# Optimization experiments

Measured on AMD Instinct MI355X. Metric: run time of the kernel, lower is better.

## Reference

```python
import jax, jax.numpy as jnp
import numpy as np

FEAT = 128 * 4 * 4   # 2048, from input_size=(64,128,4,4)
NCLS = 20            # hard-coded n_classes
S = 0.31             # threshold margin from forward()


def setup_inputs() -> dict:
    key = jax.random.key(0)
    kx, ke, kc, kf = jax.random.split(key, 4)
    x = jax.random.normal(kx, (16384, 128, 4, 4), dtype=jnp.float32)
    # encoder stub: linear 2048 -> 2048
    W_enc = jax.random.normal(ke, (FEAT, FEAT), dtype=jnp.float32) * 0.02
    b_enc = jnp.zeros((FEAT,), dtype=jnp.float32)
    # classifier: linear 2048 -> 20
    W_cls = jax.random.normal(kc, (FEAT, NCLS), dtype=jnp.float32) * 0.02
    b_cls = jnp.zeros((NCLS,), dtype=jnp.float32)
    # flow classification head: linear 2048 -> 20 (produces flow_logits)
    W_fl = jax.random.normal(kf, (FEAT, NCLS), dtype=jnp.float32) * 0.02
    b_fl = jnp.zeros((NCLS,), dtype=jnp.float32)
    return {"x": x, "W_enc": W_enc, "b_enc": b_enc,
            "W_cls": W_cls, "b_cls": b_cls, "W_fl": W_fl, "b_fl": b_fl}


def reference(x, W_enc, b_enc, W_cls, b_cls, W_fl, b_fl):
    B = x.shape[0]
    h = x.reshape(B, -1) @ W_enc + b_enc                    # encoder -> [B, 2048]
    cls_preds = jax.nn.softmax(h @ W_cls + b_cls, axis=1)   # [B, 20]
    flow_logits = h @ W_fl + b_fl                           # flow classify head, [B, 20]
    # taus = softmax(flow_logits).min(1); per-row confidence threshold
    tau = jnp.min(jax.nn.softmax(flow_logits, axis=1), axis=1)  # [B]
    predicted = jnp.max(cls_preds, axis=1)                      # [B]
    # original loop: if predicted < tau + s -> zero the row (vectorized here)
    keep = predicted >= tau + S
    return jnp.where(keep[:, None], cls_preds, jnp.zeros((), cls_preds.dtype))
```

## Files before the change

### kernel.cpp

```cpp
#include <hip/hip_runtime.h>
#include <math.h>


#define KD    2048
#define NROWS 16384
#define NCLS  20
#define NC2   40
#define SMARG 0.31f

#define WCAT_OFF 0
#define WEFF_OFF 81920
#define BIAS_OFF 163840

#define XS_STR  65
#define XS_BUF  (64 * XS_STR)
#define HACC_STR 41
#define HACC_WS  (64 * HACC_STR)
#define SMEM_FLOATS (8 * HACC_WS)

__global__ __launch_bounds__(256)
void k0_prep(const float* __restrict__ Wc, const float* __restrict__ bc,
             const float* __restrict__ Wf, const float* __restrict__ bf,
             const float* __restrict__ be, float* __restrict__ ws)
{
    const int b = blockIdx.x;
    const int t = threadIdx.x;
    if (b < 320) {
        const int idx = b * 256 + t;
        const int n = idx / NC2, c = idx % NC2;
        ws[WCAT_OFF + idx] = (c < NCLS) ? Wc[n * NCLS + c] : Wf[n * NCLS + (c - NCLS)];
        ws[WEFF_OFF + idx] = 0.f;
    } else {
        const int col = b - 320;
        const float* Wp = (col < NCLS) ? Wc : Wf;
        const int cc = (col < NCLS) ? col : col - NCLS;
        float p = 0.f;
        for (int n = t; n < KD; n += 256)
            p = fmaf(be[n], Wp[n * NCLS + cc], p);
        __shared__ float red[256];
        red[t] = p;
        __syncthreads();
        for (int s = 128; s > 0; s >>= 1) {
            if (t < s) red[t] += red[t + s];
            __syncthreads();
        }
        if (t == 0)
            ws[BIAS_OFF + col] = red[0] + ((col < NCLS) ? bc[cc] : bf[cc]);
    }
}

template<int NCHUNKS, bool FUSED>
__global__ __launch_bounds__(1024)
void skinny_gemm(const float* __restrict__ A,
                 const float* __restrict__ Bw,
                 float* __restrict__ Cacc,
                 const float* __restrict__ bias2,
                 float* __restrict__ outp)
{
    __shared__ float smem[SMEM_FLOATS];
    const int tid  = threadIdx.x;
    const int lane = tid & 63;
    const int wu   = __builtin_amdgcn_readfirstlane(tid >> 6);
    const int cgu  = wu & 1;
    const int ksu  = wu >> 1;
    const int ksub = ksu * 8;

    int m0, kbase;
    if (FUSED) { m0 = blockIdx.x * 64;        kbase = 0; }
    else       { m0 = (blockIdx.x >> 2) * 64; kbase = (blockIdx.x & 3) * (NCHUNKS * 64); }

    const int lrow = tid >> 4;
    const int lkq  = tid & 15;
    const float* aptr = A + (size_t)(m0 + lrow) * KD + kbase + 4 * lkq;

    float acc[20];
    #pragma unroll
    for (int j = 0; j < 20; ++j) acc[j] = 0.f;

    float4 v = *(const float4*)(aptr);
    {
        float* xb = smem;
        xb[(4 * lkq + 0) * XS_STR + lrow] = v.x;
        xb[(4 * lkq + 1) * XS_STR + lrow] = v.y;
        xb[(4 * lkq + 2) * XS_STR + lrow] = v.z;
        xb[(4 * lkq + 3) * XS_STR + lrow] = v.w;
    }
    __syncthreads();

    for (int c = 0; c < NCHUNKS; ++c) {
        const int buf = c & 1;
        if (c + 1 < NCHUNKS)
            v = *(const float4*)(aptr + (c + 1) * 64);

        const float* xs   = smem + buf * XS_BUF;
        const float* brow = Bw + (size_t)(kbase + c * 64 + ksub) * NC2 + 20 * cgu;
        #pragma unroll 4
        for (int kk = 0; kk < 8; ++kk) {
            float x = xs[(ksub + kk) * XS_STR + lane];
            #pragma unroll
            for (int j = 0; j < 20; ++j)
                acc[j] = fmaf(x, brow[kk * NC2 + j], acc[j]);
        }

        if (c + 1 < NCHUNKS) {
            float* xb = smem + (buf ^ 1) * XS_BUF;
            xb[(4 * lkq + 0) * XS_STR + lrow] = v.x;
            xb[(4 * lkq + 1) * XS_STR + lrow] = v.y;
            xb[(4 * lkq + 2) * XS_STR + lrow] = v.z;
            xb[(4 * lkq + 3) * XS_STR + lrow] = v.w;
        }
        __syncthreads();
    }

    float* H = smem;
    #pragma unroll
    for (int j = 0; j < 20; ++j)
        H[ksu * HACC_WS + lane * HACC_STR + 20 * cgu + j] = acc[j];
    __syncthreads();

    if (FUSED) {
        if (tid < 64) {
            float l[NC2];
            #pragma unroll
            for (int cc = 0; cc < NC2; ++cc) {
                float s = 0.f;
                #pragma unroll
                for (int ks = 0; ks < 8; ++ks)
                    s += H[ks * HACC_WS + tid * HACC_STR + cc];
                l[cc] = s + bias2[cc];
            }
            float mC = l[0];
            #pragma unroll
            for (int cc = 1; cc < NCLS; ++cc) mC = fmaxf(mC, l[cc]);
            float sC = 0.f;
            #pragma unroll
            for (int cc = 0; cc < NCLS; ++cc) sC += expf(l[cc] - mC);
            float mF = l[NCLS], mnF = l[NCLS];
            #pragma unroll
            for (int cc = NCLS + 1; cc < NC2; ++cc) {
                float vv = l[cc];
                mF = fmaxf(mF, vv);
                mnF = fminf(mnF, vv);
            }
            float sF = 0.f;
            #pragma unroll
            for (int cc = NCLS; cc < NC2; ++cc) sF += expf(l[cc] - mF);
            float pred  = 1.f / sC;
            float tau   = expf(mnF - mF) / sF;
            float scale = (pred >= tau + SMARG) ? pred : 0.f;
            float* op = outp + (size_t)(m0 + tid) * NCLS;
            #pragma unroll
            for (int cc = 0; cc < NCLS; ++cc)
                op[cc] = expf(l[cc] - mC) * scale;
        }
    } else {
        for (int idx = tid; idx < 64 * NC2; idx += 1024) {
            int row = idx / NC2, cc = idx % NC2;
            float s = 0.f;
            #pragma unroll
            for (int ks = 0; ks < 8; ++ks)
                s += H[ks * HACC_WS + row * HACC_STR + cc];
            atomicAdd(Cacc + (size_t)(m0 + row) * NC2 + cc, s);
        }
    }
}

extern "C" void kernel_launch(void* const* d_in, const int* in_sizes, int n_in,
                              void* d_out, int out_size, void* d_ws, size_t ws_size,
                              hipStream_t stream) {
    const float* X  = (const float*)d_in[0];
    const float* We = (const float*)d_in[1];
    const float* be = (const float*)d_in[2];
    const float* Wc = (const float*)d_in[3];
    const float* bc = (const float*)d_in[4];
    const float* Wf = (const float*)d_in[5];
    const float* bf = (const float*)d_in[6];
    float* out = (float*)d_out;
    float* ws  = (float*)d_ws;
    (void)in_sizes; (void)n_in; (void)out_size; (void)ws_size;

    k0_prep<<<dim3(360), dim3(256), 0, stream>>>(Wc, bc, Wf, bf, be, ws);
    skinny_gemm<8, false><<<dim3(128), dim3(1024), 0, stream>>>(
        We, ws + WCAT_OFF, ws + WEFF_OFF, nullptr, nullptr);
    skinny_gemm<32, true><<<dim3(256), dim3(1024), 0, stream>>>(
        X, ws + WEFF_OFF, nullptr, ws + BIAS_OFF, out);
}
```

Baseline: 239.6 us.

## Widen skinny GEMM chunks, use packed FMA and row-major LDS tiles

The skinny GEMM now processes 128-wide K chunks with a row-major X tile in LDS, read back as float4 vectors. Accumulation uses packed two-wide FMA on 2-float vectors. The prep kernel no longer builds a concatenated Wc/Wf copy: the first GEMM reads Wc and Wf directly through two base pointers, and the weight-fold GEMM is split 8-way over K across 256 blocks. The softmax epilogue and the output stores are vectorised. The aim is fewer LDS instructions, fewer global loads per FMA and higher FMA throughput, at the cost of more registers and a larger LDS footprint.

```diff
diff --git a/kernel.cpp b/kernel.cpp
--- a/kernel.cpp
+++ b/kernel.cpp
@@ -2,21 +2,31 @@
 #include <math.h>
 
 
+typedef float v2f __attribute__((ext_vector_type(2)));
+typedef float v4f __attribute__((ext_vector_type(4)));
+
 #define KD    2048
-#define NROWS 16384
 #define NCLS  20
 #define NC2   40
 #define SMARG 0.31f
 
-#define WCAT_OFF 0
-#define WEFF_OFF 81920
-#define BIAS_OFF 163840
-
-#define XS_STR  65
+#define WEFF_OFF 0
+#define BIAS_OFF 81920
+
+#define CHUNK   128
+#define XS_STR  132
 #define XS_BUF  (64 * XS_STR)
-#define HACC_STR 41
+#define HACC_STR 44
 #define HACC_WS  (64 * HACC_STR)
-#define SMEM_FLOATS (8 * HACC_WS)
+#define SMEM_FLOATS 22528
+
+static __device__ __forceinline__ v2f fma2(v2f a, v2f b, v2f c) {
+#if __has_builtin(__builtin_elementwise_fma)
+    return __builtin_elementwise_fma(a, b, c);
+#else
+    v2f r; r[0] = fmaf(a[0], b[0], c[0]); r[1] = fmaf(a[1], b[1], c[1]); return r;
+#endif
+}
 
 __global__ __launch_bounds__(256)
 void k0_prep(const float* __restrict__ Wc, const float* __restrict__ bc,
@@ -25,13 +35,11 @@
 {
     const int b = blockIdx.x;
     const int t = threadIdx.x;
-    if (b < 320) {
-        const int idx = b * 256 + t;
-        const int n = idx / NC2, c = idx % NC2;
-        ws[WCAT_OFF + idx] = (c < NCLS) ? Wc[n * NCLS + c] : Wf[n * NCLS + (c - NCLS)];
-        ws[WEFF_OFF + idx] = 0.f;
+    if (b < 80) {
+        v4f z = {0.f, 0.f, 0.f, 0.f};
+        *(v4f*)&ws[WEFF_OFF + 4 * (b * 256 + t)] = z;
     } else {
-        const int col = b - 320;
+        const int col = b - 80;
         const float* Wp = (col < NCLS) ? Wc : Wf;
         const int cc = (col < NCLS) ? col : col - NCLS;
         float p = 0.f;
@@ -49,109 +57,139 @@
     }
 }
 
-template<int NCHUNKS, bool FUSED>
+template<int NCHUNKS, int BSTR, bool FUSED>
 __global__ __launch_bounds__(1024)
 void skinny_gemm(const float* __restrict__ A,
-                 const float* __restrict__ Bw,
+                 const float* __restrict__ B0,
+                 const float* __restrict__ B1,
                  float* __restrict__ Cacc,
                  const float* __restrict__ bias2,
                  float* __restrict__ outp)
 {
-    __shared__ float smem[SMEM_FLOATS];
+    __shared__ __align__(16) float smem[SMEM_FLOATS];
     const int tid  = threadIdx.x;
     const int lane = tid & 63;
     const int wu   = __builtin_amdgcn_readfirstlane(tid >> 6);
     const int cgu  = wu & 1;
     const int ksu  = wu >> 1;
-    const int ksub = ksu * 8;
 
     int m0, kbase;
     if (FUSED) { m0 = blockIdx.x * 64;        kbase = 0; }
-    else       { m0 = (blockIdx.x >> 2) * 64; kbase = (blockIdx.x & 3) * (NCHUNKS * 64); }
+    else       { m0 = (blockIdx.x >> 3) * 64; kbase = (blockIdx.x & 7) * (NCHUNKS * CHUNK); }
 
     const int lrow = tid >> 4;
     const int lkq  = tid & 15;
-    const float* aptr = A + (size_t)(m0 + lrow) * KD + kbase + 4 * lkq;
-
-    float acc[20];
+    const float* aptr  = A + (size_t)(m0 + lrow) * KD + kbase + 4 * lkq;
+    const float* bbase = (cgu ? B1 : B0) + (size_t)(kbase + ksu * (CHUNK / 8)) * BSTR;
+
+    v2f acc[10];
     #pragma unroll
-    for (int j = 0; j < 20; ++j) acc[j] = 0.f;
-
-    float4 v = *(const float4*)(aptr);
+    for (int j = 0; j < 10; ++j) acc[j] = (v2f){0.f, 0.f};
+
     {
-        float* xb = smem;
-        xb[(4 * lkq + 0) * XS_STR + lrow] = v.x;
-        xb[(4 * lkq + 1) * XS_STR + lrow] = v.y;
-        xb[(4 * lkq + 2) * XS_STR + lrow] = v.z;
-        xb[(4 * lkq + 3) * XS_STR + lrow] = v.w;
+        v4f v0 = *(const v4f*)(aptr);
+        v4f v1 = *(const v4f*)(aptr + 64);
+        float* xb = smem + lrow * XS_STR;
+        *(v4f*)(xb + 4 * lkq)      = v0;
+        *(v4f*)(xb + 64 + 4 * lkq) = v1;
     }
     __syncthreads();
 
     for (int c = 0; c < NCHUNKS; ++c) {
         const int buf = c & 1;
-        if (c + 1 < NCHUNKS)
-            v = *(const float4*)(aptr + (c + 1) * 64);
-
-        const float* xs   = smem + buf * XS_BUF;
-        const float* brow = Bw + (size_t)(kbase + c * 64 + ksub) * NC2 + 20 * cgu;
-        #pragma unroll 4
-        for (int kk = 0; kk < 8; ++kk) {
-            float x = xs[(ksub + kk) * XS_STR + lane];
-            #pragma unroll
-            for (int j = 0; j < 20; ++j)
-                acc[j] = fmaf(x, brow[kk * NC2 + j], acc[j]);
-        }
-
+        v4f p0, p1;
         if (c + 1 < NCHUNKS) {
-            float* xb = smem + (buf ^ 1) * XS_BUF;
-            xb[(4 * lkq + 0) * XS_STR + lrow] = v.x;
-            xb[(4 * lkq + 1) * XS_STR + lrow] = v.y;
-            xb[(4 * lkq + 2) * XS_STR + lrow] = v.z;
-            xb[(4 * lkq + 3) * XS_STR + lrow] = v.w;
+            p0 = *(const v4f*)(aptr + (c + 1) * CHUNK);
+            p1 = *(const v4f*)(aptr + (c + 1) * CHUNK + 64);
+        }
+
+        const float* xs   = smem + buf * XS_BUF + lane * XS_STR + ksu * (CHUNK / 8);
+        const float* brow = bbase + (size_t)c * (CHUNK * BSTR);
+        #pragma unroll 2
+        for (int q = 0; q < 4; ++q) {
+            v4f xv = *(const v4f*)(xs + 4 * q);
+            #pragma unroll
+            for (int i = 0; i < 4; ++i) {
+                v2f xx = { xv[i], xv[i] };
+                const float* br = brow + (4 * q + i) * BSTR;
+                #pragma unroll
+                for (int j = 0; j < 10; ++j)
+                    acc[j] = fma2(xx, *(const v2f*)(br + 2 * j), acc[j]);
+            }
+        }
+
+        if (c + 1 < NCHUNKS) {
+            float* xb = smem + (buf ^ 1) * XS_BUF + lrow * XS_STR;
+            *(v4f*)(xb + 4 * lkq)      = p0;
+            *(v4f*)(xb + 64 + 4 * lkq) = p1;
         }
         __syncthreads();
     }
 
     float* H = smem;
-    #pragma unroll
-    for (int j = 0; j < 20; ++j)
-        H[ksu * HACC_WS + lane * HACC_STR + 20 * cgu + j] = acc[j];
+    {
+        float* Hw = H + ksu * HACC_WS + lane * HACC_STR + 20 * cgu;
+        #pragma unroll
+        for (int j = 0; j < 10; ++j)
+            *(v2f*)(Hw + 2 * j) = acc[j];
+    }
     __syncthreads();
 
     if (FUSED) {
         if (tid < 64) {
-            float l[NC2];
-            #pragma unroll
-            for (int cc = 0; cc < NC2; ++cc) {
-                float s = 0.f;
-                #pragma unroll
-                for (int ks = 0; ks < 8; ++ks)
-                    s += H[ks * HACC_WS + tid * HACC_STR + cc];
-                l[cc] = s + bias2[cc];
-            }
-            float mC = l[0];
-            #pragma unroll
-            for (int cc = 1; cc < NCLS; ++cc) mC = fmaxf(mC, l[cc]);
+            v4f l4[10];
+            #pragma unroll
+            for (int j = 0; j < 10; ++j) {
+                v4f s = *(const v4f*)(H + tid * HACC_STR + 4 * j);
+                #pragma unroll
+                for (int ks = 1; ks < 8; ++ks)
+                    s += *(const v4f*)(H + ks * HACC_WS + tid * HACC_STR + 4 * j);
+                l4[j] = s + *(const v4f*)(bias2 + 4 * j);
+            }
+            float mC = l4[0][0];
+            #pragma unroll
+            for (int j = 0; j < 5; ++j) {
+                #pragma unroll
+                for (int i = 0; i < 4; ++i) mC = fmaxf(mC, l4[j][i]);
+            }
+            float e[20];
             float sC = 0.f;
             #pragma unroll
-            for (int cc = 0; cc < NCLS; ++cc) sC += expf(l[cc] - mC);
-            float mF = l[NCLS], mnF = l[NCLS];
-            #pragma unroll
-            for (int cc = NCLS + 1; cc < NC2; ++cc) {
-                float vv = l[cc];
-                mF = fmaxf(mF, vv);
-                mnF = fminf(mnF, vv);
+            for (int j = 0; j < 5; ++j) {
+                #pragma unroll
+                for (int i = 0; i < 4; ++i) {
+                    float ev = expf(l4[j][i] - mC);
+                    e[4 * j + i] = ev;
+                    sC += ev;
+                }
+            }
+            float mF = l4[5][0], mnF = l4[5][0];
+            #pragma unroll
+            for (int j = 5; j < 10; ++j) {
+                #pragma unroll
+                for (int i = 0; i < 4; ++i) {
+                    float vv = l4[j][i];
+                    mF = fmaxf(mF, vv);
+                    mnF = fminf(mnF, vv);
+                }
             }
             float sF = 0.f;
             #pragma unroll
-            for (int cc = NCLS; cc < NC2; ++cc) sF += expf(l[cc] - mF);
+            for (int j = 5; j < 10; ++j) {
+                #pragma unroll
+                for (int i = 0; i < 4; ++i) sF += expf(l4[j][i] - mF);
+            }
             float pred  = 1.f / sC;
             float tau   = expf(mnF - mF) / sF;
             float scale = (pred >= tau + SMARG) ? pred : 0.f;
             float* op = outp + (size_t)(m0 + tid) * NCLS;
             #pragma unroll
-            for (int cc = 0; cc < NCLS; ++cc)
-                op[cc] = expf(l[cc] - mC) * scale;
+            for (int j = 0; j < 5; ++j) {
+                v4f o;
+                #pragma unroll
+                for (int i = 0; i < 4; ++i) o[i] = e[4 * j + i] * scale;
+                *(v4f*)(op + 4 * j) = o;
+            }
         }
     } else {
         for (int idx = tid; idx < 64 * NC2; idx += 1024) {
@@ -179,9 +217,9 @@
     float* ws  = (float*)d_ws;
     (void)in_sizes; (void)n_in; (void)out_size; (void)ws_size;
 
-    k0_prep<<<dim3(360), dim3(256), 0, stream>>>(Wc, bc, Wf, bf, be, ws);
-    skinny_gemm<8, false><<<dim3(128), dim3(1024), 0, stream>>>(
-        We, ws + WCAT_OFF, ws + WEFF_OFF, nullptr, nullptr);
-    skinny_gemm<32, true><<<dim3(256), dim3(1024), 0, stream>>>(
-        X, ws + WEFF_OFF, nullptr, ws + BIAS_OFF, out);
-}
+    k0_prep<<<dim3(120), dim3(256), 0, stream>>>(Wc, bc, Wf, bf, be, ws);
+    skinny_gemm<2, 20, false><<<dim3(256), dim3(1024), 0, stream>>>(
+        We, Wc, Wf, ws + WEFF_OFF, nullptr, nullptr);
+    skinny_gemm<16, 40, true><<<dim3(256), dim3(1024), 0, stream>>>(
+        X, ws + WEFF_OFF, ws + WEFF_OFF + 20, nullptr, ws + BIAS_OFF, out);
+}
```

After: 277.3 us. 1.16x slower.
